# Kernel optimization log

Hardware: AMD Instinct MI355X
Metric: run time of the kernel (lower is better)

Reference implementation:

```python
import jax, jax.numpy as jnp
import numpy as np
import math

D_MODEL = 1024
N_HEADS = 16
RANK = 16
SCALE = 16.0
T_LEN = 2048
BSZ = 2


def setup_inputs() -> dict:
    key = jax.random.key(0)
    ks = jax.random.split(key, 12)
    d, r = D_MODEL, RANK
    inp = {
        "query": jax.random.normal(ks[0], (T_LEN, BSZ, d), dtype=jnp.float32),
        "key": jax.random.normal(ks[1], (T_LEN, BSZ, d), dtype=jnp.float32),
        "value": jax.random.normal(ks[2], (T_LEN, BSZ, d), dtype=jnp.float32),
        "need_weights": 0,
        "attn_mask": 0,
        "in_proj_weight": jax.random.normal(ks[3], (3 * d, d), dtype=jnp.float32) * 0.02,
        "in_proj_bias": jax.random.normal(ks[4], (3 * d,), dtype=jnp.float32) * 0.02,
        "out_w": jax.random.normal(ks[5], (d, d), dtype=jnp.float32) * 0.02,
        "out_b": jax.random.normal(ks[6], (d,), dtype=jnp.float32) * 0.02,
        "k_a": jax.random.normal(ks[7], (r, d), dtype=jnp.float32) * 0.02,
        "k_b": jax.random.normal(ks[8], (r, d), dtype=jnp.float32) * 0.02,
        "v_a": jax.random.normal(ks[9], (r, d), dtype=jnp.float32) * 0.02,
        "v_b": jax.random.normal(ks[10], (r, d), dtype=jnp.float32) * 0.02,
    }
    return inp


def reference(query, key, value, need_weights, attn_mask,
              in_proj_weight, in_proj_bias, out_w, out_b,
              k_a, k_b, v_a, v_b):
    # NOTE: original module computes q,k,v all from `query` (self-attention);
    # `key`, `value`, `need_weights`, `attn_mask` are unused in the math.
    T, B, d = query.shape
    H = N_HEADS
    hd = d // H
    qkv = query @ in_proj_weight.T + in_proj_bias  # (T, B, 3d)
    q, k, v = jnp.split(qkv, 3, axis=-1)
    s = SCALE / RANK
    # LoRA low-rank updates on K and V (computed from query)
    k = k + s * ((query @ k_a.T) @ k_b)
    v = v + s * ((query @ v_a.T) @ v_b)
    # split heads: (T, B, H, hd)
    qh = q.reshape(T, B, H, hd)
    kh = k.reshape(T, B, H, hd)
    vh = v.reshape(T, B, H, hd)
    scale = 1.0 / math.sqrt(hd)
    scores = jnp.einsum('tbhd,sbhd->bhts', qh * scale, kh)  # (B, H, T, T)
    attn = jax.nn.softmax(scores, axis=-1)
    out = jnp.einsum('bhts,sbhd->tbhd', attn, vh).reshape(T, B, d)
    out = out @ out_w.T + out_b
    return out
```

## Files before the change

kernel.cpp:

```cpp
#include <hip/hip_runtime.h>
#include <stdint.h>

#define DEVI __device__ __forceinline__

typedef unsigned short u16;
typedef __attribute__((ext_vector_type(4))) float f32x4;
typedef __attribute__((ext_vector_type(16))) float f32x16;
typedef __attribute__((ext_vector_type(8))) short bf16x8;
typedef __attribute__((ext_vector_type(2))) unsigned int u32x2;

constexpr int T_LEN = 2048;
constexpr int BSZ   = 2;
constexpr int DM    = 1024;
constexpr int NH    = 16;
constexpr int HD    = 64;
constexpr int MROWS = T_LEN * BSZ;
constexpr float LORA_S = 16.0f / 16.0f;
constexpr float QSCALE = 0.125f * 1.4426950408889634f;

DEVI u16 f2bf(float x) {
  union { float f; uint32_t u; } v; v.f = x;
  uint32_t r = (v.u + 0x7FFFu + ((v.u >> 16) & 1u)) >> 16;
  return (u16)r;
}

DEVI uint32_t pk2bf(float a, float b) {
  return (uint32_t)f2bf(a) | ((uint32_t)f2bf(b) << 16);
}

DEVI uint32_t e2r(float x) {
  union { float f; uint32_t u; } v;
  v.f = __builtin_amdgcn_exp2f(x);
  return v.u + 0x8000u;
}

DEVI void gload_lds16(const void* g, void* l) {
  __builtin_amdgcn_global_load_lds(
      (const __attribute__((address_space(1))) void*)g,
      (__attribute__((address_space(3))) void*)l, 16, 0, 0);
}

DEVI f32x4 mfma16(bf16x8 a, bf16x8 b, f32x4 c) {
  return __builtin_amdgcn_mfma_f32_16x16x32_bf16(a, b, c, 0, 0, 0);
}
DEVI f32x16 mfma32(bf16x8 a, bf16x8 b, f32x16 c) {
  return __builtin_amdgcn_mfma_f32_32x32x16_bf16(a, b, c, 0, 0, 0);
}

DEVI int swz16(int row, int c8) { return row * 64 + ((c8 ^ (row & 7)) << 3); }

DEVI int kvswz(int rc, int l) { return rc * 128 + ((l ^ (rc & 15)) << 3); }

#define WAITBAR(N)                                        \
  do {                                                    \
    asm volatile("s_waitcnt vmcnt(" #N ")" ::: "memory"); \
    __builtin_amdgcn_sched_barrier(0);                    \
    __builtin_amdgcn_s_barrier();                         \
    __builtin_amdgcn_sched_barrier(0);                    \
  } while (0)

__global__ void prep_kernel(const float* __restrict__ query,
                            const float* __restrict__ W,
                            const float* __restrict__ ka, const float* __restrict__ kb,
                            const float* __restrict__ va, const float* __restrict__ vb,
                            const float* __restrict__ ow,
                            u16* __restrict__ Wm, u16* __restrict__ Wo,
                            u16* __restrict__ Aq) {
  const int W3 = 3 * DM * DM;
  const int WO = DM * DM;
  const int AQ = MROWS * DM;
  const int total = W3 + WO + AQ;
  for (int idx = blockIdx.x * blockDim.x + threadIdx.x; idx < total;
       idx += gridDim.x * blockDim.x) {
    if (idx < W3) {
      const int n = idx >> 10, k = idx & 1023;
      float w = W[idx];
      if (n >= 2 * DM) {
        const int n2 = n - 2 * DM;
        float a = 0.f;
#pragma unroll
        for (int r = 0; r < 16; ++r) a += va[r * DM + k] * vb[r * DM + n2];
        w += LORA_S * a;
      } else if (n >= DM) {
        const int n2 = n - DM;
        float a = 0.f;
#pragma unroll
        for (int r = 0; r < 16; ++r) a += ka[r * DM + k] * kb[r * DM + n2];
        w += LORA_S * a;
      }
      Wm[idx] = f2bf(w);
    } else if (idx < W3 + WO) {
      const int i = idx - W3;
      Wo[i] = f2bf(ow[i]);
    } else {
      const int i = idx - W3 - WO;
      Aq[i] = f2bf(query[i]);
    }
  }
}

template <int EPIL>
__global__ __launch_bounds__(256) void gemm_bt(
    const u16* __restrict__ A, const u16* __restrict__ Bt,
    const float* __restrict__ bias, float* __restrict__ Cf,
    u16* __restrict__ Qb, u16* __restrict__ Kb, u16* __restrict__ Vt,
    int M, int N, int K) {
  constexpr int BM = 128, BN = 128, BK = 64;
  __shared__ alignas(16) u16 SM[2][(BM + BN) * BK];
  const int tid = threadIdx.x;
  const int wv = tid >> 6, ln = tid & 63;
  const int l16 = ln & 15, lhi = ln >> 4;
  const int row0 = blockIdx.x * BM, col0 = blockIdx.y * BN;
  const int wr = (wv >> 1) * 64, wc = (wv & 1) * 64;

  f32x4 acc[4][4];
#pragma unroll
  for (int i = 0; i < 4; ++i)
#pragma unroll
    for (int j = 0; j < 4; ++j) acc[i][j] = f32x4{0.f, 0.f, 0.f, 0.f};

  const int srow = ln >> 3;
  const int scol = (((ln & 7) ^ (ln >> 3)) & 7) * 8;

  auto stage = [&](int buf, int ks) {
    const int k0 = ks * BK;
    u16* Al = SM[buf];
    u16* Bl = SM[buf] + BM * BK;
#pragma unroll
    for (int it = 0; it < 4; ++it) {
      const int c = wv * 4 + it;
      gload_lds16(A + (size_t)(row0 + c * 8 + srow) * K + k0 + scol, &Al[c * 512]);
      gload_lds16(Bt + (size_t)(col0 + c * 8 + srow) * K + k0 + scol, &Bl[c * 512]);
    }
  };

  const int NS = K / BK;
  stage(0, 0);
  __syncthreads();
  int cur = 0;
  for (int t = 0; t < NS; ++t) {
    if (t + 1 < NS) stage(cur ^ 1, t + 1);
    const u16* Al = SM[cur];
    const u16* Bl = SM[cur] + BM * BK;
#pragma unroll
    for (int ks = 0; ks < 2; ++ks) {
      bf16x8 af[4], bfr[4];
#pragma unroll
      for (int m = 0; m < 4; ++m)
        af[m] = *(const bf16x8*)&Al[swz16(wr + m * 16 + l16, ks * 4 + lhi)];
#pragma unroll
      for (int n = 0; n < 4; ++n)
        bfr[n] = *(const bf16x8*)&Bl[swz16(wc + n * 16 + l16, ks * 4 + lhi)];
#pragma unroll
      for (int m = 0; m < 4; ++m)
#pragma unroll
        for (int n = 0; n < 4; ++n) acc[m][n] = mfma16(af[m], bfr[n], acc[m][n]);
    }
    __syncthreads();
    cur ^= 1;
  }

  if constexpr (EPIL == 0) {
    if (col0 >= 2 * DM) {
      u16* Cl = SM[0];
#pragma unroll
      for (int m = 0; m < 4; ++m)
#pragma unroll
        for (int n = 0; n < 4; ++n) {
          const int lc = wc + n * 16 + l16;
          const float bc = bias[col0 + lc];
#pragma unroll
          for (int r = 0; r < 4; ++r) {
            const int rl = wr + m * 16 + lhi * 4 + r;
            const int tl = rl >> 1, bb = rl & 1;
            Cl[lc * 128 + bb * 64 + (((tl >> 3) ^ (lc & 7)) << 3) + (tl & 7)] =
                f2bf(acc[m][n][r] + bc);
          }
        }
      __syncthreads();
      const int h0 = (col0 - 2 * DM) >> 6;
      const int t0 = row0 >> 1;
#pragma unroll
      for (int i = 0; i < 8; ++i) {
        const int cid = i * 256 + tid;
        const int lc = cid >> 4, bb = (cid >> 3) & 1, tc = cid & 7;
        bf16x8 ch = *(const bf16x8*)&Cl[lc * 128 + bb * 64 + ((tc ^ (lc & 7)) << 3)];
        const int h = h0 + (lc >> 6), dd = lc & 63;
        *(bf16x8*)&Vt[(((size_t)(bb * NH + h)) * HD + dd) * T_LEN + t0 + tc * 8] = ch;
      }
      return;
    }
  }

#pragma unroll
  for (int m = 0; m < 4; ++m) {
#pragma unroll
    for (int n = 0; n < 4; ++n) {
      const int col = col0 + wc + n * 16 + l16;
      const float bc = bias[col];
#pragma unroll
      for (int r = 0; r < 4; ++r) {
        const int row = row0 + wr + m * 16 + lhi * 4 + r;
        const float v = acc[m][n][r] + bc;
        if constexpr (EPIL == 0) {
          const int t = row >> 1, b = row & 1;
          if (col < DM) {
            const int h = col >> 6, dd = col & 63;
            Qb[(((size_t)(b * NH + h)) * T_LEN + t) * HD + dd] = f2bf(v * QSCALE);
          } else {
            const int c2 = col - DM, h = c2 >> 6, dd = c2 & 63;
            Kb[(((size_t)(b * NH + h)) * T_LEN + t) * HD + dd] = f2bf(v);
          }
        } else {
          Cf[(size_t)row * N + col] = v;
        }
      }
    }
  }
}

__global__ __launch_bounds__(256) void attn_kernel(const u16* __restrict__ Qb,
                                                   const u16* __restrict__ Kb,
                                                   const u16* __restrict__ Vt,
                                                   u16* __restrict__ Ob) {
  constexpr int KBLK = 64;
  constexpr int NT = T_LEN / KBLK;
  __shared__ alignas(16) u16 KV[4][2][32 * 128];

  const int tid = threadIdx.x;
  const int wv = tid >> 6, ln = tid & 63;
  const int l32 = ln & 31, hi = ln >> 5;

  const int bid = blockIdx.x;
  const int lb = (bid & 7) * 64 + (bid >> 3);
  const int bh = lb >> 4;
  const int b = bh >> 4, h = bh & 15;
  const int q0 = (lb & 15) * 128 + wv * 32;

  const u16* Qh = Qb + (size_t)bh * T_LEN * HD;
  const u16* Kh = Kb + (size_t)bh * T_LEN * HD;
  const u16* Vh = Vt + (size_t)bh * HD * T_LEN;

  bf16x8 qf[4];
#pragma unroll
  for (int kd = 0; kd < 4; ++kd)
    qf[kd] = *(const bf16x8*)&Qh[(size_t)(q0 + l32) * HD + kd * 16 + hi * 8];

  bf16x8 ones;
#pragma unroll
  for (int i = 0; i < 8; ++i) ones[i] = (short)0x3F80;

  f32x16 ot[2] = {f32x16{}, f32x16{}};
  f32x16 lacc = f32x16{};

  const int g_row = ln >> 4;
  const int g_s   = ln & 15;
  const int j0 = wv * 2, j1 = wv * 2 + 1;
  const int row0r = 4 * j0 + g_row, row1r = 4 * j1 + g_row;
  const int l0 = g_s ^ (row0r & 15), l1 = g_s ^ (row1r & 15);
  const int lr0 = row0r + 32 * (l0 >> 3), lr1 = row1r + 32 * (l1 >> 3);
  const int c80 = (l0 & 7) * 8, c81 = (l1 & 7) * 8;

  const u16* ks0 = Kh + (size_t)lr0 * HD + c80;
  const u16* ks1 = Kh + (size_t)lr1 * HD + c81;
  const u16* vs0 = Vh + (size_t)lr0 * T_LEN + c80;
  const u16* vs1 = Vh + (size_t)lr1 * T_LEN + c81;

  auto stagep = [&](int buf) {
    gload_lds16(ks0, &KV[buf][0][j0 * 512]);
    gload_lds16(ks1, &KV[buf][0][j1 * 512]);
    gload_lds16(vs0, &KV[buf][1][j0 * 512]);
    gload_lds16(vs1, &KV[buf][1][j1 * 512]);
    ks0 += KBLK * HD; ks1 += KBLK * HD; vs0 += KBLK; vs1 += KBLK;
  };

  auto compute = [&](int buf) {
    const u16* Kl = KV[buf][0];
    const u16* Vl = KV[buf][1];
    f32x16 st[2] = {f32x16{}, f32x16{}};
#pragma unroll
    for (int kd = 0; kd < 4; ++kd) {
      bf16x8 k0 = *(const bf16x8*)&Kl[kvswz(l32, kd * 2 + hi)];
      bf16x8 k1 = *(const bf16x8*)&Kl[kvswz(l32, 8 + kd * 2 + hi)];
      st[0] = mfma32(k0, qf[kd], st[0]);
      st[1] = mfma32(k1, qf[kd], st[1]);
    }
    uint32_t c[2][8];
#pragma unroll
    for (int mk = 0; mk < 2; ++mk)
#pragma unroll
      for (int d = 0; d < 8; ++d)
        c[mk][d] = __builtin_amdgcn_perm(e2r(st[mk][2 * d + 1]),
                                         e2r(st[mk][2 * d]), 0x07060302u);
#pragma unroll
    for (int ksl = 0; ksl < 4; ++ksl) {
      const int mk = ksl >> 1, s2 = ksl & 1;
      uint32_t a0 = c[mk][4 * s2 + 0], b0 = c[mk][4 * s2 + 2];
      uint32_t a1 = c[mk][4 * s2 + 1], b1 = c[mk][4 * s2 + 3];
      u32x2 r0 = __builtin_amdgcn_permlane32_swap(a0, b0, false, false);
      u32x2 r1 = __builtin_amdgcn_permlane32_swap(a1, b1, false, false);
      union { bf16x8 v; uint32_t u[4]; } pu;
      pu.u[0] = r0[0]; pu.u[1] = r1[0]; pu.u[2] = r0[1]; pu.u[3] = r1[1];
      bf16x8 vf0 = *(const bf16x8*)&Vl[kvswz(l32, ksl * 2 + hi)];
      bf16x8 vf1 = *(const bf16x8*)&Vl[kvswz(l32, 8 + ksl * 2 + hi)];
      ot[0] = mfma32(vf0, pu.v, ot[0]);
      ot[1] = mfma32(vf1, pu.v, ot[1]);
      lacc = mfma32(ones, pu.v, lacc);
    }
  };

  stagep(0); stagep(1); stagep(2);

  for (int t4 = 0; t4 < NT - 4; t4 += 4) {
    WAITBAR(8); compute(0); stagep(3);
    WAITBAR(8); compute(1); stagep(0);
    WAITBAR(8); compute(2); stagep(1);
    WAITBAR(8); compute(3); stagep(2);
  }
  WAITBAR(8); compute(0); stagep(3);
  WAITBAR(8); compute(1);
  WAITBAR(4); compute(2);
  WAITBAR(0); compute(3);

  const float inv = 1.0f / lacc[0];
  const size_t rowbase = ((size_t)(q0 + l32) * BSZ + b) * DM + h * HD;
#pragma unroll
  for (int dt = 0; dt < 2; ++dt) {
#pragma unroll
    for (int g = 0; g < 4; ++g) {
      const float v0 = ot[dt][4 * g + 0] * inv;
      const float v1 = ot[dt][4 * g + 1] * inv;
      const float v2 = ot[dt][4 * g + 2] * inv;
      const float v3 = ot[dt][4 * g + 3] * inv;
      u32x2 w; w[0] = pk2bf(v0, v1); w[1] = pk2bf(v2, v3);
      const int dim = dt * 32 + 8 * g + 4 * hi;
      *(u32x2*)&Ob[rowbase + dim] = w;
    }
  }
}

extern "C" void kernel_launch(void* const* d_in, const int* in_sizes, int n_in,
                              void* d_out, int out_size, void* d_ws, size_t ws_size,
                              hipStream_t stream) {
  const float* query = (const float*)d_in[0];
  const float* W     = (const float*)d_in[5];
  const float* bias  = (const float*)d_in[6];
  const float* ow    = (const float*)d_in[7];
  const float* ob    = (const float*)d_in[8];
  const float* ka    = (const float*)d_in[9];
  const float* kb    = (const float*)d_in[10];
  const float* va    = (const float*)d_in[11];
  const float* vb    = (const float*)d_in[12];

  char* ws = (char*)d_ws;
  u16* Wm = (u16*)ws; ws += (size_t)3 * DM * DM * 2;
  u16* Wo = (u16*)ws; ws += (size_t)DM * DM * 2;
  u16* Aq = (u16*)ws; ws += (size_t)MROWS * DM * 2;
  u16* Qb = (u16*)ws; ws += (size_t)BSZ * NH * T_LEN * HD * 2;
  u16* Kb = (u16*)ws; ws += (size_t)BSZ * NH * T_LEN * HD * 2;
  u16* Vt = (u16*)ws; ws += (size_t)BSZ * NH * T_LEN * HD * 2;
  u16* Ob = (u16*)ws; ws += (size_t)MROWS * DM * 2;

  prep_kernel<<<2048, 256, 0, stream>>>(query, W, ka, kb, va, vb, ow, Wm, Wo, Aq);

  gemm_bt<0><<<dim3(MROWS / 128, (3 * DM) / 128), 256, 0, stream>>>(
      Aq, Wm, bias, nullptr, Qb, Kb, Vt, MROWS, 3 * DM, DM);

  attn_kernel<<<512, 256, 0, stream>>>(Qb, Kb, Vt, Ob);

  gemm_bt<1><<<dim3(MROWS / 128, DM / 128), 256, 0, stream>>>(
      Ob, Wo, ob, (float*)d_out, nullptr, nullptr, nullptr, MROWS, DM, DM);
}
```

Measured before the change: 115.4 us.

## Deepen GEMM LDS pipeline to four stages with smaller K tiles

Result: faster. 110.4 us (-4.3%).

```diff
diff --git a/kernel.cpp b/kernel.cpp
--- a/kernel.cpp
+++ b/kernel.cpp
@@ -46,8 +46,6 @@
 DEVI f32x16 mfma32(bf16x8 a, bf16x8 b, f32x16 c) {
   return __builtin_amdgcn_mfma_f32_32x32x16_bf16(a, b, c, 0, 0, 0);
 }
-
-DEVI int swz16(int row, int c8) { return row * 64 + ((c8 ^ (row & 7)) << 3); }
 
 DEVI int kvswz(int rc, int l) { return rc * 128 + ((l ^ (rc & 15)) << 3); }
 
@@ -105,8 +103,8 @@
     const float* __restrict__ bias, float* __restrict__ Cf,
     u16* __restrict__ Qb, u16* __restrict__ Kb, u16* __restrict__ Vt,
     int M, int N, int K) {
-  constexpr int BM = 128, BN = 128, BK = 64;
-  __shared__ alignas(16) u16 SM[2][(BM + BN) * BK];
+  constexpr int BM = 128, BN = 128, BK = 32;
+  __shared__ alignas(16) u16 SM[4][2][4096];
   const int tid = threadIdx.x;
   const int wv = tid >> 6, ln = tid & 63;
   const int l16 = ln & 15, lhi = ln >> 4;
@@ -119,50 +117,66 @@
 #pragma unroll
     for (int j = 0; j < 4; ++j) acc[i][j] = f32x4{0.f, 0.f, 0.f, 0.f};
 
-  const int srow = ln >> 3;
-  const int scol = (((ln & 7) ^ (ln >> 3)) & 7) * 8;
-
-  auto stage = [&](int buf, int ks) {
-    const int k0 = ks * BK;
-    u16* Al = SM[buf];
-    u16* Bl = SM[buf] + BM * BK;
-#pragma unroll
-    for (int it = 0; it < 4; ++it) {
-      const int c = wv * 4 + it;
-      gload_lds16(A + (size_t)(row0 + c * 8 + srow) * K + k0 + scol, &Al[c * 512]);
-      gload_lds16(Bt + (size_t)(col0 + c * 8 + srow) * K + k0 + scol, &Bl[c * 512]);
-    }
+  const int lrA = wv * 16 + (ln >> 3);
+  const int lrB = lrA + 8;
+  const int s_ = ln & 7;
+  const int la = s_ ^ (lrA & 7), lb = s_ ^ (lrB & 7);
+  const int ra = lrA + 64 * (la >> 2), ca = (la & 3) * 8;
+  const int rb = lrB + 64 * (lb >> 2), cb = (lb & 3) * 8;
+
+  const u16* pa0 = A + (size_t)(row0 + ra) * K + ca;
+  const u16* pa1 = A + (size_t)(row0 + rb) * K + cb;
+  const u16* pb0 = Bt + (size_t)(col0 + ra) * K + ca;
+  const u16* pb1 = Bt + (size_t)(col0 + rb) * K + cb;
+
+  auto stagep = [&](int buf) {
+    gload_lds16(pa0, &SM[buf][0][(wv * 16) * 64]);
+    gload_lds16(pa1, &SM[buf][0][(wv * 16 + 8) * 64]);
+    gload_lds16(pb0, &SM[buf][1][(wv * 16) * 64]);
+    gload_lds16(pb1, &SM[buf][1][(wv * 16 + 8) * 64]);
+    pa0 += BK; pa1 += BK; pb0 += BK; pb1 += BK;
   };
 
+  auto compute = [&](int buf) {
+    const u16* Al = SM[buf][0];
+    const u16* Bl = SM[buf][1];
+    bf16x8 af[4], bfr[4];
+#pragma unroll
+    for (int m = 0; m < 4; ++m) {
+      const int r = wr + m * 16 + l16, lr = r & 63;
+      const int sl = (lhi | ((r >> 6) << 2)) ^ (lr & 7);
+      af[m] = *(const bf16x8*)&Al[lr * 64 + sl * 8];
+    }
+#pragma unroll
+    for (int n = 0; n < 4; ++n) {
+      const int r = wc + n * 16 + l16, lr = r & 63;
+      const int sl = (lhi | ((r >> 6) << 2)) ^ (lr & 7);
+      bfr[n] = *(const bf16x8*)&Bl[lr * 64 + sl * 8];
+    }
+#pragma unroll
+    for (int m = 0; m < 4; ++m)
+#pragma unroll
+      for (int n = 0; n < 4; ++n) acc[m][n] = mfma16(af[m], bfr[n], acc[m][n]);
+  };
+
   const int NS = K / BK;
-  stage(0, 0);
-  __syncthreads();
-  int cur = 0;
-  for (int t = 0; t < NS; ++t) {
-    if (t + 1 < NS) stage(cur ^ 1, t + 1);
-    const u16* Al = SM[cur];
-    const u16* Bl = SM[cur] + BM * BK;
-#pragma unroll
-    for (int ks = 0; ks < 2; ++ks) {
-      bf16x8 af[4], bfr[4];
-#pragma unroll
-      for (int m = 0; m < 4; ++m)
-        af[m] = *(const bf16x8*)&Al[swz16(wr + m * 16 + l16, ks * 4 + lhi)];
-#pragma unroll
-      for (int n = 0; n < 4; ++n)
-        bfr[n] = *(const bf16x8*)&Bl[swz16(wc + n * 16 + l16, ks * 4 + lhi)];
-#pragma unroll
-      for (int m = 0; m < 4; ++m)
-#pragma unroll
-        for (int n = 0; n < 4; ++n) acc[m][n] = mfma16(af[m], bfr[n], acc[m][n]);
-    }
-    __syncthreads();
-    cur ^= 1;
-  }
+  stagep(0); stagep(1); stagep(2);
+
+  for (int t4 = 0; t4 < NS - 4; t4 += 4) {
+    WAITBAR(8); compute(0); stagep(3);
+    WAITBAR(8); compute(1); stagep(0);
+    WAITBAR(8); compute(2); stagep(1);
+    WAITBAR(8); compute(3); stagep(2);
+  }
+  WAITBAR(8); compute(0); stagep(3);
+  WAITBAR(8); compute(1);
+  WAITBAR(4); compute(2);
+  WAITBAR(0); compute(3);
 
   if constexpr (EPIL == 0) {
     if (col0 >= 2 * DM) {
-      u16* Cl = SM[0];
+      u16* Cl = (u16*)SM;
+      __syncthreads();
 #pragma unroll
       for (int m = 0; m < 4; ++m)
 #pragma unroll
```
